# Optimization experiments

Hardware: AMD Instinct MI355X
Metric: run time of the kernel (lower is better)

Reference implementation:

```python
import jax, jax.numpy as jnp
import numpy as np

B = 65536  # batch size


def setup_inputs() -> dict:
    key = jax.random.key(0)
    ks = jax.random.split(key, 8)
    x = jax.random.normal(ks[0], (B, 784), dtype=jnp.float32)
    conv_w = jax.random.normal(ks[1], (3, 3), dtype=jnp.float32)
    w1 = jax.random.normal(ks[2], (676, 256), dtype=jnp.float32) * 0.04
    b1 = jnp.zeros((256,), dtype=jnp.float32)
    w2 = jax.random.normal(ks[3], (256, 128), dtype=jnp.float32) * 0.06
    b2 = jnp.zeros((128,), dtype=jnp.float32)
    w3 = jax.random.normal(ks[4], (128, 10), dtype=jnp.float32) * 0.09
    b3 = jnp.zeros((10,), dtype=jnp.float32)
    return {"x": x, "conv_w": conv_w, "w1": w1, "b1": b1,
            "w2": w2, "b2": b2, "w3": w3, "b3": b3}


def reference(x, conv_w, w1, b1, w2, b2, w3, b3):
    # x: [B, 784] -> images [B, 1, 28, 28]
    img = x.reshape(-1, 1, 28, 28)
    # Convolve() is a valid cross-correlation (tensordot of window with kernel,
    # no flip) -> lax.conv_general_dilated (also no kernel flip).
    kern = conv_w.reshape(1, 1, 3, 3)  # [O, I, kh, kw]
    y = jax.lax.conv_general_dilated(
        img, kern, window_strides=(1, 1), padding="VALID",
        dimension_numbers=("NCHW", "OIHW", "NCHW"))  # [B, 1, 26, 26]
    h = y.reshape(y.shape[0], 26 * 26)
    h = jax.nn.relu(h @ w1 + b1)
    h = jax.nn.relu(h @ w2 + b2)
    return h @ w3 + b3  # [B, 10] logits
```

## Files before the change

kernel.cpp:

```cpp
#include <hip/hip_runtime.h>
#include <hip/hip_bf16.h>
#include <stdint.h>

typedef __bf16 bf16x8 __attribute__((ext_vector_type(8)));
typedef float  f32x4  __attribute__((ext_vector_type(4)));

#define PIN4(v) asm volatile("" :: "v"((v).x), "v"((v).y), "v"((v).z), "v"((v).w))

#define B_ROWS 65536
#define KC1 22
#define KC2 8
#define KC3 4
#define H1S 264
#define H2S 136
#define PANEL_B 16384
#define W1B_ELEMS (704*256)
#define W2B_ELEMS (256*128)
#define W3B_ELEMS (128*16)
#define W1B_BYTES (KC1*PANEL_B)
#define WS_WEIGHTS (W1B_BYTES + W2B_ELEMS*2 + W3B_ELEMS*2)
#define H0B_BYTES ((size_t)B_ROWS*704*2)
#define GM 64

#define MR 32
#define H0S 712

__global__ void pack_weights(const float* __restrict__ w1,
                             const float* __restrict__ w2,
                             const float* __restrict__ w3,
                             __hip_bfloat16* __restrict__ w1b,
                             __hip_bfloat16* __restrict__ w2b,
                             __hip_bfloat16* __restrict__ w3b) {
    int idx = blockIdx.x * 256 + threadIdx.x;
    if (idx < W1B_ELEMS) {
        int ki = idx & 31, t = idx >> 5;
        int n = t & 255, kc = t >> 8;
        int k = kc * 32 + ki;
        float v = (k < 676) ? w1[k * 256 + n] : 0.0f;
        int gg = ki >> 3, j = ki & 7;
        int u = n * 4 + (gg ^ (n & 3));
        *(__hip_bfloat16*)((char*)w1b + (size_t)kc * PANEL_B + u * 16 + j * 2)
            = __float2bfloat16(v);
    } else if (idx < W1B_ELEMS + W2B_ELEMS) {
        int j = idx - W1B_ELEMS;
        int ki = j & 31, t = j >> 5;
        int n = t & 127, kc = t >> 7;
        w2b[j] = __float2bfloat16(w2[(kc * 32 + ki) * 128 + n]);
    } else if (idx < W1B_ELEMS + W2B_ELEMS + W3B_ELEMS) {
        int j = idx - W1B_ELEMS - W2B_ELEMS;
        int ki = j & 31, t = j >> 5;
        int n = t & 15, kc = t >> 4;
        float v = (n < 10) ? w3[(kc * 32 + ki) * 10 + n] : 0.0f;
        w3b[j] = __float2bfloat16(v);
    }
}

template<int S>
__device__ __forceinline__ void conv_body(
        const float* __restrict__ xr, __hip_bfloat16* __restrict__ hp,
        float c00, float c01, float c02, float c10, float c11, float c12,
        float c20, float c21, float c22) {
    float4 v[3][4];
    #pragma unroll
    for (int d = 0; d < 3; d++) {
        const float4* p4 = (const float4*)(xr + d * 28);
        #pragma unroll
        for (int q = 0; q < 4; q++) v[d][q] = p4[S * 3 + q];
    }
    #pragma unroll
    for (int d = 0; d < 3; d++)
        #pragma unroll
        for (int q = 0; q < 4; q++) PIN4(v[d][q]);
    float rb[3][16];
    #pragma unroll
    for (int d = 0; d < 3; d++)
        #pragma unroll
        for (int q = 0; q < 4; q++) {
            rb[d][q*4+0] = v[d][q].x; rb[d][q*4+1] = v[d][q].y;
            rb[d][q*4+2] = v[d][q].z; rb[d][q*4+3] = v[d][q].w;
        }
    #pragma unroll
    for (int jj = 0; jj < 13; jj++) {
        float a = c00*rb[0][S+jj] + c01*rb[0][S+jj+1] + c02*rb[0][S+jj+2]
                + c10*rb[1][S+jj] + c11*rb[1][S+jj+1] + c12*rb[1][S+jj+2]
                + c20*rb[2][S+jj] + c21*rb[2][S+jj+1] + c22*rb[2][S+jj+2];
        hp[jj] = __float2bfloat16(a);
    }
}

__global__ __launch_bounds__(256, 4)
void conv_kernel(const float* __restrict__ x, const float* __restrict__ cw,
                 __hip_bfloat16* __restrict__ h0b) {
    const int tid  = threadIdx.x;
    const int half = tid >> 7;
    const int u    = blockIdx.x * 128 + (tid & 127);
    const int i    = u % 26;
    const int r    = u / 26;
    const float c00 = cw[0], c01 = cw[1], c02 = cw[2];
    const float c10 = cw[3], c11 = cw[4], c12 = cw[5];
    const float c20 = cw[6], c21 = cw[7], c22 = cw[8];
    const float* xr = x + (size_t)r * 784 + i * 28;
    __hip_bfloat16* hp = h0b + (size_t)r * 704 + i * 26 + half * 13;
    if (half == 0) conv_body<0>(xr, hp, c00, c01, c02, c10, c11, c12, c20, c21, c22);
    else           conv_body<1>(xr, hp, c00, c01, c02, c10, c11, c12, c20, c21, c22);
    if (half == 1 && i == 25) {
        uint* pz = (uint*)(h0b + (size_t)r * 704 + 676);
        #pragma unroll
        for (int q = 0; q < 14; q++) pz[q] = 0u;
    }
}

__global__ __launch_bounds__(256, 2)
void gemm_kernel(const __hip_bfloat16* __restrict__ h0b,
                 const __hip_bfloat16* __restrict__ w1b, const float* __restrict__ b1,
                 const __hip_bfloat16* __restrict__ w2b, const float* __restrict__ b2,
                 const __hip_bfloat16* __restrict__ w3b, const float* __restrict__ b3,
                 float* __restrict__ out) {
    __shared__ __align__(16) char smem[8192 + 32768 + GM * H1S * 2];
    char* astg = smem;
    char* bstg = smem + 8192;
    __hip_bfloat16* h1s = (__hip_bfloat16*)(smem + 40960);
    __hip_bfloat16* h2s = (__hip_bfloat16*)smem;

    const int tid  = threadIdx.x;
    const int r0   = blockIdx.x * GM;
    const int wave = tid >> 6;
    const int lane = tid & 63;
    const int l15  = lane & 15;
    const int g    = lane >> 4;
    const int mh   = wave >> 1;
    const int nh   = wave & 1;
    const int swg  = (g ^ (l15 & 3)) * 16;

    {
        f32x4 acc[2][8];
        #pragma unroll
        for (int mt = 0; mt < 2; mt++)
            #pragma unroll
            for (int nt = 0; nt < 8; nt++)
                acc[mt][nt] = (f32x4){0.f, 0.f, 0.f, 0.f};

        const int srow = tid >> 2, sgx = tid & 3;
        const __hip_bfloat16* asrc = h0b + (size_t)(r0 + srow) * 704
                                         + (sgx ^ (srow & 3)) * 8;
        const char* bsrc = (const char*)w1b;

        __builtin_amdgcn_global_load_lds((const uint32_t*)asrc,
            (uint32_t*)(astg + wave * 1024), 16, 0, 0);
        #pragma unroll
        for (int j2 = 0; j2 < 4; j2++)
            __builtin_amdgcn_global_load_lds(
                (const uint32_t*)(bsrc + j2 * 4096 + tid * 16),
                (uint32_t*)(bstg + j2 * 4096 + wave * 1024), 16, 0, 0);
        __syncthreads();

        for (int kc = 0; kc < KC1; kc++) {
            const int cur = kc & 1;
            if (kc + 1 < KC1) {
                __builtin_amdgcn_global_load_lds(
                    (const uint32_t*)(asrc + (kc + 1) * 32),
                    (uint32_t*)(astg + (cur ^ 1) * 4096 + wave * 1024), 16, 0, 0);
                #pragma unroll
                for (int j2 = 0; j2 < 4; j2++)
                    __builtin_amdgcn_global_load_lds(
                        (const uint32_t*)(bsrc + (size_t)(kc + 1) * PANEL_B + j2 * 4096 + tid * 16),
                        (uint32_t*)(bstg + (cur ^ 1) * 16384 + j2 * 4096 + wave * 1024), 16, 0, 0);
            }
            bf16x8 av[2], bv[8];
            #pragma unroll
            for (int mt = 0; mt < 2; mt++)
                av[mt] = *(const bf16x8*)(astg + cur * 4096
                            + (mh * 32 + mt * 16 + l15) * 64 + swg);
            #pragma unroll
            for (int nt = 0; nt < 8; nt++)
                bv[nt] = *(const bf16x8*)(bstg + cur * 16384
                            + (nh * 128 + nt * 16 + l15) * 64 + swg);
            #pragma unroll
            for (int mt = 0; mt < 2; mt++)
                #pragma unroll
                for (int nt = 0; nt < 8; nt++)
                    acc[mt][nt] = __builtin_amdgcn_mfma_f32_16x16x32_bf16(
                        av[mt], bv[nt], acc[mt][nt], 0, 0, 0);
            __syncthreads();
        }
        #pragma unroll
        for (int nt = 0; nt < 8; nt++) {
            const int n = nh * 128 + nt * 16 + l15;
            const float bias = b1[n];
            #pragma unroll
            for (int mt = 0; mt < 2; mt++) {
                #pragma unroll
                for (int q = 0; q < 4; q++) {
                    const int row = mh * 32 + mt * 16 + g * 4 + q;
                    float v = acc[mt][nt][q] + bias;
                    h1s[row * H1S + n] = __float2bfloat16(fmaxf(v, 0.0f));
                }
            }
        }
    }
    __syncthreads();

    {
        f32x4 acc[2][4];
        #pragma unroll
        for (int mt = 0; mt < 2; mt++)
            #pragma unroll
            for (int nt = 0; nt < 4; nt++)
                acc[mt][nt] = (f32x4){0.f, 0.f, 0.f, 0.f};
        const int nb = nh * 64;
        bf16x8 bb2[3][4];
        #pragma unroll
        for (int p = 0; p < 2; p++)
            #pragma unroll
            for (int nt = 0; nt < 4; nt++)
                bb2[p][nt] = *(const bf16x8*)(w2b + ((p * 128 + nb + nt * 16 + l15) * 32 + g * 8));
        #pragma unroll
        for (int kc = 0; kc < KC2; kc++) {
            const int cur = kc % 3, nxt = (kc + 2) % 3;
            if (kc + 2 < KC2) {
                #pragma unroll
                for (int nt = 0; nt < 4; nt++)
                    bb2[nxt][nt] = *(const bf16x8*)(w2b + (((kc + 2) * 128 + nb + nt * 16 + l15) * 32 + g * 8));
            }
            bf16x8 ab[2];
            #pragma unroll
            for (int mt = 0; mt < 2; mt++)
                ab[mt] = *(const bf16x8*)(h1s + (mh * 32 + mt * 16 + l15) * H1S + kc * 32 + g * 8);
            #pragma unroll
            for (int mt = 0; mt < 2; mt++)
                #pragma unroll
                for (int nt = 0; nt < 4; nt++)
                    acc[mt][nt] = __builtin_amdgcn_mfma_f32_16x16x32_bf16(
                        ab[mt], bb2[cur][nt], acc[mt][nt], 0, 0, 0);
        }
        #pragma unroll
        for (int nt = 0; nt < 4; nt++) {
            const int n = nb + nt * 16 + l15;
            const float bias = b2[n];
            #pragma unroll
            for (int mt = 0; mt < 2; mt++) {
                #pragma unroll
                for (int q = 0; q < 4; q++) {
                    const int row = mh * 32 + mt * 16 + g * 4 + q;
                    float v = acc[mt][nt][q] + bias;
                    h2s[row * H2S + n] = __float2bfloat16(fmaxf(v, 0.0f));
                }
            }
        }
    }
    __syncthreads();

    {
        f32x4 acc3 = (f32x4){0.f, 0.f, 0.f, 0.f};
        #pragma unroll
        for (int kc = 0; kc < KC3; kc++) {
            bf16x8 a = *(const bf16x8*)(h2s + (wave * 16 + l15) * H2S + kc * 32 + g * 8);
            bf16x8 b = *(const bf16x8*)(w3b + ((kc * 16 + l15) * 32 + g * 8));
            acc3 = __builtin_amdgcn_mfma_f32_16x16x32_bf16(a, b, acc3, 0, 0, 0);
        }
        if (l15 < 10) {
            const float bias = b3[l15];
            #pragma unroll
            for (int q = 0; q < 4; q++) {
                const int row = wave * 16 + g * 4 + q;
                out[(size_t)(r0 + row) * 10 + l15] = acc3[q] + bias;
            }
        }
    }
}

__global__ __launch_bounds__(256, 2)
void fused_model(const float* __restrict__ x, const float* __restrict__ cw,
                 const __hip_bfloat16* __restrict__ w1b, const float* __restrict__ b1,
                 const __hip_bfloat16* __restrict__ w2b, const float* __restrict__ b2,
                 const __hip_bfloat16* __restrict__ w3b, const float* __restrict__ b3,
                 float* __restrict__ out) {
    __shared__ __align__(16) char smem[MR * H0S * 2 + MR * H1S * 2];
    __hip_bfloat16* h0s = (__hip_bfloat16*)smem;
    __hip_bfloat16* h1s = (__hip_bfloat16*)(smem + MR * H0S * 2);
    __hip_bfloat16* h2s = (__hip_bfloat16*)smem;
    const char* w1c = (const char*)w1b;

    const int tid = threadIdx.x;
    const int r0  = blockIdx.x * MR;

    const float c00 = cw[0], c01 = cw[1], c02 = cw[2];
    const float c10 = cw[3], c11 = cw[4], c12 = cw[5];
    const float c20 = cw[6], c21 = cw[7], c22 = cw[8];

    for (int t = tid; t < MR * 26; t += 256) {
        int r = t / 26;
        int i = t - r * 26;
        const float* xr = x + (size_t)(r0 + r) * 784 + i * 28;
        float4 v[21];
        #pragma unroll
        for (int di = 0; di < 3; di++) {
            const float4* p4 = (const float4*)(xr + di * 28);
            #pragma unroll
            for (int q = 0; q < 7; q++) v[di * 7 + q] = p4[q];
        }
        #pragma unroll
        for (int k = 0; k < 21; k++) PIN4(v[k]);
        float rb[3][28];
        #pragma unroll
        for (int di = 0; di < 3; di++) {
            #pragma unroll
            for (int q = 0; q < 7; q++) {
                rb[di][q*4+0] = v[di*7+q].x; rb[di][q*4+1] = v[di*7+q].y;
                rb[di][q*4+2] = v[di*7+q].z; rb[di][q*4+3] = v[di*7+q].w;
            }
        }
        __hip_bfloat162* hp = (__hip_bfloat162*)(h0s + r * H0S + i * 26);
        #pragma unroll
        for (int k = 0; k < 13; k++) {
            const int j0 = 2 * k, j1 = 2 * k + 1;
            float a0 = c00*rb[0][j0] + c01*rb[0][j0+1] + c02*rb[0][j0+2]
                     + c10*rb[1][j0] + c11*rb[1][j0+1] + c12*rb[1][j0+2]
                     + c20*rb[2][j0] + c21*rb[2][j0+1] + c22*rb[2][j0+2];
            float a1 = c00*rb[0][j1] + c01*rb[0][j1+1] + c02*rb[0][j1+2]
                     + c10*rb[1][j1] + c11*rb[1][j1+1] + c12*rb[1][j1+2]
                     + c20*rb[2][j1] + c21*rb[2][j1+1] + c22*rb[2][j1+2];
            __hip_bfloat162 pr;
            pr.x = __float2bfloat16(a0);
            pr.y = __float2bfloat16(a1);
            hp[k] = pr;
        }
    }
    for (int t = tid; t < MR * 18; t += 256) {
        int r = t / 18;
        int c = t - r * 18;
        ((uint*)(h0s + r * H0S + 676))[c] = 0u;
    }
    __syncthreads();

    const int wave = tid >> 6;
    const int lane = tid & 63;
    const int l15  = lane & 15;
    const int g    = lane >> 4;
    const int swg  = (g ^ (l15 & 3)) * 16;

    {
        f32x4 acc[2][4];
        #pragma unroll
        for (int mt = 0; mt < 2; mt++)
            #pragma unroll
            for (int nt = 0; nt < 4; nt++)
                acc[mt][nt] = (f32x4){0.f, 0.f, 0.f, 0.f};
        const int nb = wave * 64;
        bf16x8 ab[3][2], bb[3][4];
        #pragma unroll
        for (int p = 0; p < 2; p++) {
            #pragma unroll
            for (int mt = 0; mt < 2; mt++)
                ab[p][mt] = *(const bf16x8*)(h0s + (mt * 16 + l15) * H0S + p * 32 + g * 8);
            #pragma unroll
            for (int nt = 0; nt < 4; nt++) {
                const int n = nb + nt * 16 + l15;
                bb[p][nt] = *(const bf16x8*)(w1c + (size_t)p * PANEL_B + n * 64 + swg);
            }
        }
        #pragma unroll
        for (int kc = 0; kc < KC1; kc++) {
            const int cur = kc % 3;
            const int nxt = (kc + 2) % 3;
            if (kc + 2 < KC1) {
                #pragma unroll
                for (int mt = 0; mt < 2; mt++)
                    ab[nxt][mt] = *(const bf16x8*)(h0s + (mt * 16 + l15) * H0S + (kc + 2) * 32 + g * 8);
                #pragma unroll
                for (int nt = 0; nt < 4; nt++) {
                    const int n = nb + nt * 16 + l15;
                    bb[nxt][nt] = *(const bf16x8*)(w1c + (size_t)(kc + 2) * PANEL_B + n * 64 + swg);
                }
            }
            #pragma unroll
            for (int mt = 0; mt < 2; mt++)
                #pragma unroll
                for (int nt = 0; nt < 4; nt++)
                    acc[mt][nt] = __builtin_amdgcn_mfma_f32_16x16x32_bf16(
                        ab[cur][mt], bb[cur][nt], acc[mt][nt], 0, 0, 0);
        }
        #pragma unroll
        for (int nt = 0; nt < 4; nt++) {
            const int n = nb + nt * 16 + l15;
            const float bias = b1[n];
            #pragma unroll
            for (int mt = 0; mt < 2; mt++) {
                #pragma unroll
                for (int q = 0; q < 4; q++) {
                    const int row = mt * 16 + g * 4 + q;
                    float v = acc[mt][nt][q] + bias;
                    h1s[row * H1S + n] = __float2bfloat16(fmaxf(v, 0.0f));
                }
            }
        }
    }
    __syncthreads();

    {
        f32x4 acc[2][2];
        #pragma unroll
        for (int mt = 0; mt < 2; mt++)
            #pragma unroll
            for (int nt = 0; nt < 2; nt++)
                acc[mt][nt] = (f32x4){0.f, 0.f, 0.f, 0.f};
        const int nb = wave * 32;
        bf16x8 ab[3][2], bb[3][2];
        #pragma unroll
        for (int p = 0; p < 2; p++) {
            #pragma unroll
            for (int mt = 0; mt < 2; mt++)
                ab[p][mt] = *(const bf16x8*)(h1s + (mt * 16 + l15) * H1S + p * 32 + g * 8);
            #pragma unroll
            for (int nt = 0; nt < 2; nt++)
                bb[p][nt] = *(const bf16x8*)(w2b + ((p * 128 + nb + nt * 16 + l15) * 32 + g * 8));
        }
        #pragma unroll
        for (int kc = 0; kc < KC2; kc++) {
            const int cur = kc % 3;
            const int nxt = (kc + 2) % 3;
            if (kc + 2 < KC2) {
                #pragma unroll
                for (int mt = 0; mt < 2; mt++)
                    ab[nxt][mt] = *(const bf16x8*)(h1s + (mt * 16 + l15) * H1S + (kc + 2) * 32 + g * 8);
                #pragma unroll
                for (int nt = 0; nt < 2; nt++)
                    bb[nxt][nt] = *(const bf16x8*)(w2b + (((kc + 2) * 128 + nb + nt * 16 + l15) * 32 + g * 8));
            }
            #pragma unroll
            for (int mt = 0; mt < 2; mt++)
                #pragma unroll
                for (int nt = 0; nt < 2; nt++)
                    acc[mt][nt] = __builtin_amdgcn_mfma_f32_16x16x32_bf16(
                        ab[cur][mt], bb[cur][nt], acc[mt][nt], 0, 0, 0);
        }
        #pragma unroll
        for (int nt = 0; nt < 2; nt++) {
            const int n = nb + nt * 16 + l15;
            const float bias = b2[n];
            #pragma unroll
            for (int mt = 0; mt < 2; mt++) {
                #pragma unroll
                for (int q = 0; q < 4; q++) {
                    const int row = mt * 16 + g * 4 + q;
                    float v = acc[mt][nt][q] + bias;
                    h2s[row * H2S + n] = __float2bfloat16(fmaxf(v, 0.0f));
                }
            }
        }
    }
    __syncthreads();

    if (wave < 2) {
        f32x4 acc3 = (f32x4){0.f, 0.f, 0.f, 0.f};
        #pragma unroll
        for (int kc = 0; kc < KC3; kc++) {
            bf16x8 a = *(const bf16x8*)(h2s + (wave * 16 + l15) * H2S + kc * 32 + g * 8);
            bf16x8 b = *(const bf16x8*)(w3b + ((kc * 16 + l15) * 32 + g * 8));
            acc3 = __builtin_amdgcn_mfma_f32_16x16x32_bf16(a, b, acc3, 0, 0, 0);
        }
        if (l15 < 10) {
            const float bias = b3[l15];
            #pragma unroll
            for (int q = 0; q < 4; q++) {
                const int row = wave * 16 + g * 4 + q;
                out[(size_t)(r0 + row) * 10 + l15] = acc3[q] + bias;
            }
        }
    }
}

extern "C" void kernel_launch(void* const* d_in, const int* in_sizes, int n_in,
                              void* d_out, int out_size, void* d_ws, size_t ws_size,
                              hipStream_t stream) {
    const float* x  = (const float*)d_in[0];
    const float* cw = (const float*)d_in[1];
    const float* w1 = (const float*)d_in[2];
    const float* b1 = (const float*)d_in[3];
    const float* w2 = (const float*)d_in[4];
    const float* b2 = (const float*)d_in[5];
    const float* w3 = (const float*)d_in[6];
    const float* b3 = (const float*)d_in[7];
    float* out = (float*)d_out;

    __hip_bfloat16* w1b = (__hip_bfloat16*)d_ws;
    __hip_bfloat16* w2b = (__hip_bfloat16*)((char*)d_ws + W1B_BYTES);
    __hip_bfloat16* w3b = w2b + W2B_ELEMS;

    const int pack_total = W1B_ELEMS + W2B_ELEMS + W3B_ELEMS;
    pack_weights<<<(pack_total + 255) / 256, 256, 0, stream>>>(w1, w2, w3, w1b, w2b, w3b);

    const size_t need = (size_t)WS_WEIGHTS + H0B_BYTES;
    if (ws_size >= need) {
        __hip_bfloat16* h0b = (__hip_bfloat16*)((char*)d_ws + WS_WEIGHTS);
        conv_kernel<<<B_ROWS * 26 / 128, 256, 0, stream>>>(x, cw, h0b);
        gemm_kernel<<<B_ROWS / GM, 256, 0, stream>>>(h0b, w1b, b1, w2b, b2, w3b, b3, out);
    } else {
        fused_model<<<B_ROWS / MR, 256, 0, stream>>>(x, cw, w1b, b1, w2b, b2, w3b, b3, out);
    }
}
```

Baseline: 381.0 us.

## Pad conv rows to 32, use 8-wave GEMM blocks, repack W1

The conv kernel now has one thread per output row. It writes each 26-wide row padded to 32 bf16 using vector stores, so h0b grows to 832 columns and each K chunk of layer 1 lines up with one image row. W1 is repacked to match that padded layout and gains an extra linear copy for the fallback fused kernel. The GEMM kernel moves from 4 waves to 8 waves per block, each wave covering a quarter of N, which cuts per-wave accumulators and is meant to raise latency hiding. The cost is about 18% more layer-1 K work and more intermediate traffic to write and read back.

```diff
diff --git a/kernel.cpp b/kernel.cpp
--- a/kernel.cpp
+++ b/kernel.cpp
@@ -4,50 +4,66 @@
 
 typedef __bf16 bf16x8 __attribute__((ext_vector_type(8)));
 typedef float  f32x4  __attribute__((ext_vector_type(4)));
+typedef unsigned short ushort8 __attribute__((ext_vector_type(8)));
 
 #define PIN4(v) asm volatile("" :: "v"((v).x), "v"((v).y), "v"((v).z), "v"((v).w))
 
 #define B_ROWS 65536
-#define KC1 22
+#define KC1 26
+#define KC1F 22
 #define KC2 8
 #define KC3 4
 #define H1S 264
 #define H2S 136
 #define PANEL_B 16384
-#define W1B_ELEMS (704*256)
+#define W1SW_ELEMS (KC1*256*32)
+#define W1LIN_ELEMS (704*256)
 #define W2B_ELEMS (256*128)
 #define W3B_ELEMS (128*16)
-#define W1B_BYTES (KC1*PANEL_B)
-#define WS_WEIGHTS (W1B_BYTES + W2B_ELEMS*2 + W3B_ELEMS*2)
-#define H0B_BYTES ((size_t)B_ROWS*704*2)
+#define W1SW_BYTES (KC1*PANEL_B)
+#define W1LIN_BYTES (W1LIN_ELEMS*2)
+#define WS_WEIGHTS (W1SW_BYTES + W1LIN_BYTES + W2B_ELEMS*2 + W3B_ELEMS*2)
+#define H0B_ELEMS ((size_t)B_ROWS*832)
+#define H0B_BYTES (H0B_ELEMS*2)
 #define GM 64
 
 #define MR 32
 #define H0S 712
+
+__device__ __forceinline__ unsigned short f2b(float f) {
+    __hip_bfloat16 h = __float2bfloat16(f);
+    return *reinterpret_cast<unsigned short*>(&h);
+}
 
 __global__ void pack_weights(const float* __restrict__ w1,
                              const float* __restrict__ w2,
                              const float* __restrict__ w3,
-                             __hip_bfloat16* __restrict__ w1b,
+                             __hip_bfloat16* __restrict__ w1sw,
+                             __hip_bfloat16* __restrict__ w1lin,
                              __hip_bfloat16* __restrict__ w2b,
                              __hip_bfloat16* __restrict__ w3b) {
     int idx = blockIdx.x * 256 + threadIdx.x;
-    if (idx < W1B_ELEMS) {
+    if (idx < W1SW_ELEMS) {
         int ki = idx & 31, t = idx >> 5;
+        int n = t & 255, kc = t >> 8;
+        float v = (ki < 26) ? w1[(kc * 26 + ki) * 256 + n] : 0.0f;
+        size_t byte = (size_t)kc * PANEL_B
+                    + (size_t)(n * 4 + ((ki >> 3) ^ (n & 3))) * 16 + (ki & 7) * 2;
+        *(__hip_bfloat16*)((char*)w1sw + byte) = __float2bfloat16(v);
+    } else if (idx < W1SW_ELEMS + W1LIN_ELEMS) {
+        int j = idx - W1SW_ELEMS;
+        int ki = j & 31, t = j >> 5;
         int n = t & 255, kc = t >> 8;
         int k = kc * 32 + ki;
         float v = (k < 676) ? w1[k * 256 + n] : 0.0f;
-        int gg = ki >> 3, j = ki & 7;
-        int u = n * 4 + (gg ^ (n & 3));
-        *(__hip_bfloat16*)((char*)w1b + (size_t)kc * PANEL_B + u * 16 + j * 2)
-            = __float2bfloat16(v);
-    } else if (idx < W1B_ELEMS + W2B_ELEMS) {
-        int j = idx - W1B_ELEMS;
+        w1lin[j] = __float2bfloat16(v);
+    } else if (idx < W1SW_ELEMS + W1LIN_ELEMS + W2B_ELEMS) {
+        int j = idx - W1SW_ELEMS - W1LIN_ELEMS;
         int ki = j & 31, t = j >> 5;
         int n = t & 127, kc = t >> 7;
         w2b[j] = __float2bfloat16(w2[(kc * 32 + ki) * 128 + n]);
-    } else if (idx < W1B_ELEMS + W2B_ELEMS + W3B_ELEMS) {
-        int j = idx - W1B_ELEMS - W2B_ELEMS;
+    } else if (idx < W1SW_ELEMS + W1LIN_ELEMS + W2B_ELEMS + W3B_ELEMS) {
+        int j = idx - W1SW_ELEMS - W1LIN_ELEMS - W2B_ELEMS;
         int ki = j & 31, t = j >> 5;
         int n = t & 15, kc = t >> 4;
         float v = (n < 10) ? w3[(kc * 32 + ki) * 10 + n] : 0.0f;
@@ -55,64 +71,56 @@
     }
 }
 
-template<int S>
-__device__ __forceinline__ void conv_body(
-        const float* __restrict__ xr, __hip_bfloat16* __restrict__ hp,
-        float c00, float c01, float c02, float c10, float c11, float c12,
-        float c20, float c21, float c22) {
-    float4 v[3][4];
-    #pragma unroll
-    for (int d = 0; d < 3; d++) {
-        const float4* p4 = (const float4*)(xr + d * 28);
-        #pragma unroll
-        for (int q = 0; q < 4; q++) v[d][q] = p4[S * 3 + q];
-    }
-    #pragma unroll
-    for (int d = 0; d < 3; d++)
-        #pragma unroll
-        for (int q = 0; q < 4; q++) PIN4(v[d][q]);
-    float rb[3][16];
-    #pragma unroll
-    for (int d = 0; d < 3; d++)
-        #pragma unroll
-        for (int q = 0; q < 4; q++) {
-            rb[d][q*4+0] = v[d][q].x; rb[d][q*4+1] = v[d][q].y;
-            rb[d][q*4+2] = v[d][q].z; rb[d][q*4+3] = v[d][q].w;
-        }
-    #pragma unroll
-    for (int jj = 0; jj < 13; jj++) {
-        float a = c00*rb[0][S+jj] + c01*rb[0][S+jj+1] + c02*rb[0][S+jj+2]
-                + c10*rb[1][S+jj] + c11*rb[1][S+jj+1] + c12*rb[1][S+jj+2]
-                + c20*rb[2][S+jj] + c21*rb[2][S+jj+1] + c22*rb[2][S+jj+2];
-        hp[jj] = __float2bfloat16(a);
-    }
-}
-
-__global__ __launch_bounds__(256, 4)
+__global__ __launch_bounds__(256, 2)
 void conv_kernel(const float* __restrict__ x, const float* __restrict__ cw,
                  __hip_bfloat16* __restrict__ h0b) {
-    const int tid  = threadIdx.x;
-    const int half = tid >> 7;
-    const int u    = blockIdx.x * 128 + (tid & 127);
-    const int i    = u % 26;
-    const int r    = u / 26;
+    const int u = blockIdx.x * 256 + threadIdx.x;
+    const int r = u / 26;
+    const int i = u - r * 26;
     const float c00 = cw[0], c01 = cw[1], c02 = cw[2];
     const float c10 = cw[3], c11 = cw[4], c12 = cw[5];
     const float c20 = cw[6], c21 = cw[7], c22 = cw[8];
     const float* xr = x + (size_t)r * 784 + i * 28;
-    __hip_bfloat16* hp = h0b + (size_t)r * 704 + i * 26 + half * 13;
-    if (half == 0) conv_body<0>(xr, hp, c00, c01, c02, c10, c11, c12, c20, c21, c22);
-    else           conv_body<1>(xr, hp, c00, c01, c02, c10, c11, c12, c20, c21, c22);
-    if (half == 1 && i == 25) {
-        uint* pz = (uint*)(h0b + (size_t)r * 704 + 676);
-        #pragma unroll
-        for (int q = 0; q < 14; q++) pz[q] = 0u;
-    }
+
+    float4 v[3][7];
+    #pragma unroll
+    for (int d = 0; d < 3; d++) {
+        const float4* p4 = (const float4*)(xr + d * 28);
+        #pragma unroll
+        for (int q = 0; q < 7; q++) v[d][q] = p4[q];
+    }
+    #pragma unroll
+    for (int d = 0; d < 3; d++)
+        #pragma unroll
+        for (int q = 0; q < 7; q++) PIN4(v[d][q]);
+
+    float rb[3][28];
+    #pragma unroll
+    for (int d = 0; d < 3; d++)
+        #pragma unroll
+        for (int q = 0; q < 7; q++) {
+            rb[d][q*4+0] = v[d][q].x; rb[d][q*4+1] = v[d][q].y;
+            rb[d][q*4+2] = v[d][q].z; rb[d][q*4+3] = v[d][q].w;
+        }
+    ushort8 o[4];
+    #pragma unroll
+    for (int jj = 0; jj < 26; jj++) {
+        float a = c00*rb[0][jj] + c01*rb[0][jj+1] + c02*rb[0][jj+2]
+                + c10*rb[1][jj] + c11*rb[1][jj+1] + c12*rb[1][jj+2]
+                + c20*rb[2][jj] + c21*rb[2][jj+1] + c22*rb[2][jj+2];
+        o[jj >> 3][jj & 7] = f2b(a);
+    }
+    #pragma unroll
+    for (int jj = 26; jj < 32; jj++) o[3][jj & 7] = 0;
+
+    unsigned short* hp = (unsigned short*)(h0b + (size_t)r * 832 + i * 32);
+    #pragma unroll
+    for (int q = 0; q < 4; q++) *(ushort8*)(hp + q * 8) = o[q];
 }
 
-__global__ __launch_bounds__(256, 2)
+__global__ __launch_bounds__(512, 4)
 void gemm_kernel(const __hip_bfloat16* __restrict__ h0b,
-                 const __hip_bfloat16* __restrict__ w1b, const float* __restrict__ b1,
+                 const __hip_bfloat16* __restrict__ w1sw, const float* __restrict__ b1,
                  const __hip_bfloat16* __restrict__ w2b, const float* __restrict__ b2,
                  const __hip_bfloat16* __restrict__ w3b, const float* __restrict__ b3,
                  float* __restrict__ out) {
@@ -128,64 +136,66 @@
     const int lane = tid & 63;
     const int l15  = lane & 15;
     const int g    = lane >> 4;
-    const int mh   = wave >> 1;
-    const int nh   = wave & 1;
+    const int mh   = wave >> 2;
+    const int nq   = wave & 3;
     const int swg  = (g ^ (l15 & 3)) * 16;
 
     {
-        f32x4 acc[2][8];
+        f32x4 acc[2][4];
         #pragma unroll
         for (int mt = 0; mt < 2; mt++)
             #pragma unroll
-            for (int nt = 0; nt < 8; nt++)
+            for (int nt = 0; nt < 4; nt++)
                 acc[mt][nt] = (f32x4){0.f, 0.f, 0.f, 0.f};
 
         const int srow = tid >> 2, sgx = tid & 3;
-        const __hip_bfloat16* asrc = h0b + (size_t)(r0 + srow) * 704
+        const __hip_bfloat16* asrc = h0b + (size_t)(r0 + srow) * 832
                                          + (sgx ^ (srow & 3)) * 8;
-        const char* bsrc = (const char*)w1b;
-
-        __builtin_amdgcn_global_load_lds((const uint32_t*)asrc,
-            (uint32_t*)(astg + wave * 1024), 16, 0, 0);
-        #pragma unroll
-        for (int j2 = 0; j2 < 4; j2++)
+        const char* bsrc = (const char*)w1sw;
+
+        if (tid < 256)
+            __builtin_amdgcn_global_load_lds((const uint32_t*)asrc,
+                (uint32_t*)(astg + wave * 1024), 16, 0, 0);
+        #pragma unroll
+        for (int j2 = 0; j2 < 2; j2++)
             __builtin_amdgcn_global_load_lds(
-                (const uint32_t*)(bsrc + j2 * 4096 + tid * 16),
-                (uint32_t*)(bstg + j2 * 4096 + wave * 1024), 16, 0, 0);
+                (const uint32_t*)(bsrc + j2 * 8192 + tid * 16),
+                (uint32_t*)(bstg + j2 * 8192 + wave * 1024), 16, 0, 0);
         __syncthreads();
 
         for (int kc = 0; kc < KC1; kc++) {
             const int cur = kc & 1;
             if (kc + 1 < KC1) {
-                __builtin_amdgcn_global_load_lds(
-                    (const uint32_t*)(asrc + (kc + 1) * 32),
-                    (uint32_t*)(astg + (cur ^ 1) * 4096 + wave * 1024), 16, 0, 0);
-                #pragma unroll
-                for (int j2 = 0; j2 < 4; j2++)
+                if (tid < 256)
                     __builtin_amdgcn_global_load_lds(
-                        (const uint32_t*)(bsrc + (size_t)(kc + 1) * PANEL_B + j2 * 4096 + tid * 16),
-                        (uint32_t*)(bstg + (cur ^ 1) * 16384 + j2 * 4096 + wave * 1024), 16, 0, 0);
-            }
-            bf16x8 av[2], bv[8];
+                        (const uint32_t*)(asrc + (kc + 1) * 32),
+                        (uint32_t*)(astg + (cur ^ 1) * 4096 + wave * 1024), 16, 0, 0);
+                #pragma unroll
+                for (int j2 = 0; j2 < 2; j2++)
+                    __builtin_amdgcn_global_load_lds(
+                        (const uint32_t*)(bsrc + (size_t)(kc + 1) * PANEL_B + j2 * 8192 + tid * 16),
+                        (uint32_t*)(bstg + (cur ^ 1) * 16384 + j2 * 8192 + wave * 1024), 16, 0, 0);
+            }
+            bf16x8 av[2], bv[4];
             #pragma unroll
             for (int mt = 0; mt < 2; mt++)
                 av[mt] = *(const bf16x8*)(astg + cur * 4096
                             + (mh * 32 + mt * 16 + l15) * 64 + swg);
             #pragma unroll
-            for (int nt = 0; nt < 8; nt++)
+            for (int nt = 0; nt < 4; nt++)
                 bv[nt] = *(const bf16x8*)(bstg + cur * 16384
-                            + (nh * 128 + nt * 16 + l15) * 64 + swg);
-            #pragma unroll
-            for (int mt = 0; mt < 2; mt++)
-                #pragma unroll
-                for (int nt = 0; nt < 8; nt++)
+                            + (nq * 64 + nt * 16 + l15) * 64 + swg);
+            #pragma unroll
+            for (int mt = 0; mt < 2; mt++)
+                #pragma unroll
+                for (int nt = 0; nt < 4; nt++)
                     acc[mt][nt] = __builtin_amdgcn_mfma_f32_16x16x32_bf16(
                         av[mt], bv[nt], acc[mt][nt], 0, 0, 0);
             __syncthreads();
         }
         #pragma unroll
-        for (int nt = 0; nt < 8; nt++) {
-            const int n = nh * 128 + nt * 16 + l15;
+        for (int nt = 0; nt < 4; nt++) {
+            const int n = nq * 64 + nt * 16 + l15;
             const float bias = b1[n];
             #pragma unroll
             for (int mt = 0; mt < 2; mt++) {
@@ -201,25 +211,25 @@
     __syncthreads();
 
     {
-        f32x4 acc[2][4];
+        f32x4 acc[2][2];
         #pragma unroll
         for (int mt = 0; mt < 2; mt++)
             #pragma unroll
-            for (int nt = 0; nt < 4; nt++)
+            for (int nt = 0; nt < 2; nt++)
                 acc[mt][nt] = (f32x4){0.f, 0.f, 0.f, 0.f};
-        const int nb = nh * 64;
-        bf16x8 bb2[3][4];
+        const int nb = nq * 32;
+        bf16x8 bb2[3][2];
         #pragma unroll
         for (int p = 0; p < 2; p++)
             #pragma unroll
-            for (int nt = 0; nt < 4; nt++)
+            for (int nt = 0; nt < 2; nt++)
                 bb2[p][nt] = *(const bf16x8*)(w2b + ((p * 128 + nb + nt * 16 + l15) * 32 + g * 8));
         #pragma unroll
         for (int kc = 0; kc < KC2; kc++) {
             const int cur = kc % 3, nxt = (kc + 2) % 3;
             if (kc + 2 < KC2) {
                 #pragma unroll
-                for (int nt = 0; nt < 4; nt++)
+                for (int nt = 0; nt < 2; nt++)
                     bb2[nxt][nt] = *(const bf16x8*)(w2b + (((kc + 2) * 128 + nb + nt * 16 + l15) * 32 + g * 8));
             }
             bf16x8 ab[2];
@@ -229,12 +239,12 @@
             #pragma unroll
             for (int mt = 0; mt < 2; mt++)
                 #pragma unroll
-                for (int nt = 0; nt < 4; nt++)
+                for (int nt = 0; nt < 2; nt++)
                     acc[mt][nt] = __builtin_amdgcn_mfma_f32_16x16x32_bf16(
                         ab[mt], bb2[cur][nt], acc[mt][nt], 0, 0, 0);
         }
         #pragma unroll
-        for (int nt = 0; nt < 4; nt++) {
+        for (int nt = 0; nt < 2; nt++) {
             const int n = nb + nt * 16 + l15;
             const float bias = b2[n];
             #pragma unroll
@@ -250,7 +260,7 @@
     }
     __syncthreads();
 
-    {
+    if (wave < 4) {
         f32x4 acc3 = (f32x4){0.f, 0.f, 0.f, 0.f};
         #pragma unroll
         for (int kc = 0; kc < KC3; kc++) {
@@ -279,7 +289,6 @@
     __hip_bfloat16* h0s = (__hip_bfloat16*)smem;
     __hip_bfloat16* h1s = (__hip_bfloat16*)(smem + MR * H0S * 2);
     __hip_bfloat16* h2s = (__hip_bfloat16*)smem;
-    const char* w1c = (const char*)w1b;
 
     const int tid = threadIdx.x;
     const int r0  = blockIdx.x * MR;
@@ -337,7 +346,6 @@
     const int lane = tid & 63;
     const int l15  = lane & 15;
     const int g    = lane >> 4;
-    const int swg  = (g ^ (l15 & 3)) * 16;
 
     {
         f32x4 acc[2][4];
@@ -354,24 +362,20 @@
             for (int mt = 0; mt < 2; mt++)
                 ab[p][mt] = *(const bf16x8*)(h0s + (mt * 16 + l15) * H0S + p * 32 + g * 8);
             #pragma unroll
-            for (int nt = 0; nt < 4; nt++) {
-                const int n = nb + nt * 16 + l15;
-                bb[p][nt] = *(const bf16x8*)(w1c + (size_t)p * PANEL_B + n * 64 + swg);
-            }
-        }
-        #pragma unroll
-        for (int kc = 0; kc < KC1; kc++) {
+            for (int nt = 0; nt < 4; nt++)
+                bb[p][nt] = *(const bf16x8*)(w1b + ((p * 256 + nb + nt * 16 + l15) * 32 + g * 8));
+        }
+        #pragma unroll
+        for (int kc = 0; kc < KC1F; kc++) {
             const int cur = kc % 3;
             const int nxt = (kc + 2) % 3;
-            if (kc + 2 < KC1) {
+            if (kc + 2 < KC1F) {
                 #pragma unroll
                 for (int mt = 0; mt < 2; mt++)
                     ab[nxt][mt] = *(const bf16x8*)(h0s + (mt * 16 + l15) * H0S + (kc + 2) * 32 + g * 8);
                 #pragma unroll
-                for (int nt = 0; nt < 4; nt++) {
-                    const int n = nb + nt * 16 + l15;
-                    bb[nxt][nt] = *(const bf16x8*)(w1c + (size_t)(kc + 2) * PANEL_B + n * 64 + swg);
-                }
+                for (int nt = 0; nt < 4; nt++)
+                    bb[nxt][nt] = *(const bf16x8*)(w1b + (((kc + 2) * 256 + nb + nt * 16 + l15) * 32 + g * 8));
             }
             #pragma unroll
             for (int mt = 0; mt < 2; mt++)
@@ -483,19 +487,21 @@
     const float* b3 = (const float*)d_in[7];
     float* out = (float*)d_out;
 
-    __hip_bfloat16* w1b = (__hip_bfloat16*)d_ws;
-    __hip_bfloat16* w2b = (__hip_bfloat16*)((char*)d_ws + W1B_BYTES);
-    __hip_bfloat16* w3b = w2b + W2B_ELEMS;
-
-    const int pack_total = W1B_ELEMS + W2B_ELEMS + W3B_ELEMS;
-    pack_weights<<<(pack_total + 255) / 256, 256, 0, stream>>>(w1, w2, w3, w1b, w2b, w3b);
+    __hip_bfloat16* w1sw  = (__hip_bfloat16*)d_ws;
+    __hip_bfloat16* w1lin = (__hip_bfloat16*)((char*)d_ws + W1SW_BYTES);
+    __hip_bfloat16* w2b   = (__hip_bfloat16*)((char*)d_ws + W1SW_BYTES + W1LIN_BYTES);
+    __hip_bfloat16* w3b   = w2b + W2B_ELEMS;
+
+    const int pack_total = W1SW_ELEMS + W1LIN_ELEMS + W2B_ELEMS + W3B_ELEMS;
+    pack_weights<<<(pack_total + 255) / 256, 256, 0, stream>>>(
+        w1, w2, w3, w1sw, w1lin, w2b, w3b);
 
     const size_t need = (size_t)WS_WEIGHTS + H0B_BYTES;
     if (ws_size >= need) {
         __hip_bfloat16* h0b = (__hip_bfloat16*)((char*)d_ws + WS_WEIGHTS);
-        conv_kernel<<<B_ROWS * 26 / 128, 256, 0, stream>>>(x, cw, h0b);
-        gemm_kernel<<<B_ROWS / GM, 256, 0, stream>>>(h0b, w1b, b1, w2b, b2, w3b, b3, out);
+        conv_kernel<<<B_ROWS * 26 / 256, 256, 0, stream>>>(x, cw, h0b);
+        gemm_kernel<<<B_ROWS / GM, 512, 0, stream>>>(h0b, w1sw, b1, w2b, b2, w3b, b3, out);
     } else {
-        fused_model<<<B_ROWS / MR, 256, 0, stream>>>(x, cw, w1b, b1, w2b, b2, w3b, b3, out);
+        fused_model<<<B_ROWS / MR, 256, 0, stream>>>(x, cw, w1lin, b1, w2b, b2, w3b, b3, out);
     }
 }
```

After: 379.0 us. No clear change (-0.5%).
